# Kernel tuning notes

Hardware: AMD Instinct MI355X
Metric: run time of the kernel (lower is better)

Reference implementation:

```python
import jax, jax.numpy as jnp
import numpy as np

B, C, M = 4, 4096, 2048
H, D = 16, 128
S = D // 2


def setup_inputs() -> dict:
    key = jax.random.key(0)
    k1, k2, k3, k4 = jax.random.split(key, 4)
    x = jax.random.normal(k1, (B, C, M), dtype=jnp.float32)
    q = jax.random.normal(k2, (B, H, C, D), dtype=jnp.float32)
    k = jax.random.normal(k3, (B, H, C, D), dtype=jnp.float32)
    embed_weight = jax.random.normal(k4, (H, M), dtype=jnp.float32)
    pos_weight = jnp.ones((H,), dtype=jnp.float32)
    # buffer: theta = 10000 ** (-arange(0, D, 2) / D), shape [S]
    theta_steps = jnp.power(10000.0, -jnp.arange(0, D, 2, dtype=jnp.float32) / D)
    return {"x": x, "q": q, "k": k, "embed_weight": embed_weight,
            "pos_weight": pos_weight, "theta_steps": theta_steps}


def _rotate(proj_BHCD, cos_BHCS, sin_BHCS):
    # Givens matrix per (b,h,c,s): [[cos, sin], [-sin, cos]], applied as
    # rot_j = sum_i G[i,j] * p_i  =>  r0 = cos*p0 - sin*p1 ; r1 = sin*p0 + cos*p1
    Bs, Hs, Cs, Ds = proj_BHCD.shape
    p = proj_BHCD.reshape(Bs, Hs, Cs, Ds // 2, 2)
    p0, p1 = p[..., 0], p[..., 1]
    r0 = cos_BHCS * p0 - sin_BHCS * p1
    r1 = sin_BHCS * p0 + cos_BHCS * p1
    return jnp.stack([r0, r1], axis=-1).reshape(Bs, Hs, Cs, Ds)


def reference(x, q, k, embed_weight, pos_weight, theta_steps):
    # data-dependent position: input_BHC = x @ embed_weight per head
    input_BHC = jnp.einsum('bcm,hm->bhc', x, embed_weight)
    Cn = x.shape[1]
    pos_BHC = pos_weight[None, :, None] * jnp.arange(Cn, dtype=x.dtype) + input_BHC
    ang_BHCS = pos_BHC[..., None] * theta_steps  # [B,H,C,S]
    cos_t, sin_t = jnp.cos(ang_BHCS), jnp.sin(ang_BHCS)
    rot_q = _rotate(q, cos_t, sin_t)
    rot_k = _rotate(k, cos_t, sin_t)
    return jnp.stack([rot_q, rot_k], axis=0)  # [2,B,H,C,D]
```

## Files before the change

kernel.cpp:

```cpp
#include <hip/hip_runtime.h>

#define Bn 4
#define Cn 4096
#define Mn 2048
#define Hn 16
#define Dn 128
#define Sn 64

typedef float f4 __attribute__((ext_vector_type(4)));

__global__ __launch_bounds__(1024, 4) void pos_kernel(
    const float* __restrict__ x,
    const float* __restrict__ W,
    const float* __restrict__ pw,
    float* __restrict__ pos)
{
    __shared__ __align__(16) float Wl[Hn * Mn];
    __shared__ float posbuf[Hn][33];

    const int t = threadIdx.x;

    const float4* W4  = (const float4*)W;
    float4*       Wl4 = (float4*)Wl;
#pragma unroll
    for (int kk = 0; kk < 8; ++kk)
        Wl4[kk * 1024 + t] = W4[kk * 1024 + t];
    __syncthreads();

    const int wid  = t >> 6;
    const int lane = t & 63;
    const int row0 = blockIdx.x * 32;
    const int b    = row0 >> 12;
    const int c0   = row0 & 4095;
    const int r0   = row0 + wid * 2;

    const float4* x4 = (const float4*)x;
    const size_t  xb = (size_t)r0 * (Mn / 4);

    float acc0[16], acc1[16];
#pragma unroll
    for (int h = 0; h < Hn; ++h) { acc0[h] = 0.0f; acc1[h] = 0.0f; }

    float4 xa = x4[xb + lane];
    float4 xc = x4[xb + 512 + lane];
#pragma unroll
    for (int j = 0; j < 8; ++j) {
        float4 na, nc;
        if (j < 7) {
            na = x4[xb + (j + 1) * 64 + lane];
            nc = x4[xb + 512 + (j + 1) * 64 + lane];
        }
#pragma unroll
        for (int h = 0; h < Hn; ++h) {
            const float4 wv = Wl4[h * 512 + j * 64 + lane];
            acc0[h] += xa.x * wv.x; acc0[h] += xa.y * wv.y;
            acc0[h] += xa.z * wv.z; acc0[h] += xa.w * wv.w;
            acc1[h] += xc.x * wv.x; acc1[h] += xc.y * wv.y;
            acc1[h] += xc.z * wv.z; acc1[h] += xc.w * wv.w;
        }
        if (j < 7) { xa = na; xc = nc; }
    }

    float vals[32];
#pragma unroll
    for (int h = 0; h < Hn; ++h) { vals[h] = acc0[h]; vals[16 + h] = acc1[h]; }

#pragma unroll
    for (int s = 0; s < 5; ++s) {
        const int m = 1 << s;
        const int nout = 16 >> s;
        const bool up = (lane & m) != 0;
#pragma unroll
        for (int k = 0; k < 16; ++k) {
            if (k < nout) {
                float a = vals[2 * k], bb = vals[2 * k + 1];
                float mine = up ? bb : a;
                float oth  = up ? a  : bb;
                vals[k] = mine + __shfl_xor(oth, m);
            }
        }
    }
    const float tot = vals[0] + __shfl_xor(vals[0], 32);

    if (lane < 32) {
        const int h = lane & 15;
        const int r = (lane >> 4) & 1;
        posbuf[h][wid * 2 + r] = tot;
    }
    __syncthreads();

    if (t < 512) {
        const int h  = t >> 5;
        const int cc = t & 31;
        const int c  = c0 + cc;
        pos[((size_t)(b * Hn + h)) * Cn + c] = pw[h] * (float)c + posbuf[h][cc];
    }
}

__global__ __launch_bounds__(256) void rot_kernel(
    const float* __restrict__ q,
    const float* __restrict__ k,
    const float* __restrict__ theta,
    const float* __restrict__ pos,
    float* __restrict__ out)
{
    const size_t tid = (size_t)blockIdx.x * 256 + threadIdx.x;
    const int sp = (int)(tid & 31);
    const size_t row = tid >> 5;

    const float p = pos[row];
    const float2 th = ((const float2*)theta)[sp];

    constexpr float inv2pi = 0.15915494309189535f;
    float r0 = p * th.x * inv2pi;
    float r1 = p * th.y * inv2pi;
    r0 = r0 - floorf(r0);
    r1 = r1 - floorf(r1);
    const float cs0 = __builtin_amdgcn_cosf(r0);
    const float sn0 = __builtin_amdgcn_sinf(r0);
    const float cs1 = __builtin_amdgcn_cosf(r1);
    const float sn1 = __builtin_amdgcn_sinf(r1);

    const f4* q4 = (const f4*)q;
    const f4* k4 = (const f4*)k;
    f4* o4 = (f4*)out;
    const size_t idx = row * 32 + sp;
    const size_t half = (size_t)Bn * Hn * Cn * 32;

    const f4 qv = q4[idx];
    f4 ov;
    ov.x = cs0 * qv.x - sn0 * qv.y;
    ov.y = sn0 * qv.x + cs0 * qv.y;
    ov.z = cs1 * qv.z - sn1 * qv.w;
    ov.w = sn1 * qv.z + cs1 * qv.w;
    __builtin_nontemporal_store(ov, o4 + idx);

    const f4 kv = k4[idx];
    f4 ok;
    ok.x = cs0 * kv.x - sn0 * kv.y;
    ok.y = sn0 * kv.x + cs0 * kv.y;
    ok.z = cs1 * kv.z - sn1 * kv.w;
    ok.w = sn1 * kv.z + cs1 * kv.w;
    __builtin_nontemporal_store(ok, o4 + idx + half);
}

extern "C" void kernel_launch(void* const* d_in, const int* in_sizes, int n_in,
                              void* d_out, int out_size, void* d_ws, size_t ws_size,
                              hipStream_t stream) {
    const float* x     = (const float*)d_in[0];
    const float* q     = (const float*)d_in[1];
    const float* k     = (const float*)d_in[2];
    const float* W     = (const float*)d_in[3];
    const float* pw    = (const float*)d_in[4];
    const float* theta = (const float*)d_in[5];
    float* out = (float*)d_out;
    float* pos = (float*)d_ws;

    pos_kernel<<<512, 1024, 0, stream>>>(x, W, pw, pos);

    rot_kernel<<<32768, 256, 0, stream>>>(q, k, theta, pos, out);
}
```

Before: 553.2 us.

## Process four rows per wavefront in pos kernel and halve block count

Each wavefront in the position-projection kernel now handles four x rows instead of two, so each shared-memory W read feeds four rows. The grid is halved, which halves the number of times the 128KB W matrix is staged into LDS. The W layout in LDS is rearranged to be j-major, and the shuffle reduction is extended by one stage so it covers 64 values. The cost is more accumulator registers, which can reduce occupancy, and fewer blocks (256) to spread across the CUs.

```diff
diff --git a/kernel.cpp b/kernel.cpp
--- a/kernel.cpp
+++ b/kernel.cpp
@@ -16,62 +16,82 @@
     float* __restrict__ pos)
 {
     __shared__ __align__(16) float Wl[Hn * Mn];
-    __shared__ float posbuf[Hn][33];
+    __shared__ float posbuf[Hn][65];
 
     const int t = threadIdx.x;
 
     const float4* W4  = (const float4*)W;
     float4*       Wl4 = (float4*)Wl;
 #pragma unroll
-    for (int kk = 0; kk < 8; ++kk)
-        Wl4[kk * 1024 + t] = W4[kk * 1024 + t];
+    for (int kk = 0; kk < 8; ++kk) {
+        const int idx = kk * 1024 + t;
+        const int h   = idx >> 9;
+        const int m4  = idx & 511;
+        const int j   = m4 >> 6;
+        const int ln  = m4 & 63;
+        Wl4[(j * 16 + h) * 64 + ln] = W4[idx];
+    }
     __syncthreads();
 
     const int wid  = t >> 6;
     const int lane = t & 63;
-    const int row0 = blockIdx.x * 32;
+    const int row0 = blockIdx.x * 64;
     const int b    = row0 >> 12;
     const int c0   = row0 & 4095;
-    const int r0   = row0 + wid * 2;
+    const int r0   = row0 + wid * 4;
 
     const float4* x4 = (const float4*)x;
     const size_t  xb = (size_t)r0 * (Mn / 4);
 
-    float acc0[16], acc1[16];
+    float acc[4][16];
 #pragma unroll
-    for (int h = 0; h < Hn; ++h) { acc0[h] = 0.0f; acc1[h] = 0.0f; }
+    for (int r = 0; r < 4; ++r)
+#pragma unroll
+        for (int h = 0; h < Hn; ++h) acc[r][h] = 0.0f;
 
-    float4 xa = x4[xb + lane];
-    float4 xc = x4[xb + 512 + lane];
+    float4 cur[4];
+#pragma unroll
+    for (int r = 0; r < 4; ++r) cur[r] = x4[xb + (size_t)r * 512 + lane];
+
 #pragma unroll
     for (int j = 0; j < 8; ++j) {
-        float4 na, nc;
+        float4 nxt[4];
         if (j < 7) {
-            na = x4[xb + (j + 1) * 64 + lane];
-            nc = x4[xb + 512 + (j + 1) * 64 + lane];
+#pragma unroll
+            for (int r = 0; r < 4; ++r)
+                nxt[r] = x4[xb + (size_t)r * 512 + (j + 1) * 64 + lane];
         }
+        const float4* wj = Wl4 + j * 1024;
 #pragma unroll
         for (int h = 0; h < Hn; ++h) {
-            const float4 wv = Wl4[h * 512 + j * 64 + lane];
-            acc0[h] += xa.x * wv.x; acc0[h] += xa.y * wv.y;
-            acc0[h] += xa.z * wv.z; acc0[h] += xa.w * wv.w;
-            acc1[h] += xc.x * wv.x; acc1[h] += xc.y * wv.y;
-            acc1[h] += xc.z * wv.z; acc1[h] += xc.w * wv.w;
+            const float4 wv = wj[h * 64 + lane];
+#pragma unroll
+            for (int r = 0; r < 4; ++r) {
+                acc[r][h] += cur[r].x * wv.x;
+                acc[r][h] += cur[r].y * wv.y;
+                acc[r][h] += cur[r].z * wv.z;
+                acc[r][h] += cur[r].w * wv.w;
+            }
         }
-        if (j < 7) { xa = na; xc = nc; }
+        if (j < 7) {
+#pragma unroll
+            for (int r = 0; r < 4; ++r) cur[r] = nxt[r];
+        }
     }
 
-    float vals[32];
+    float vals[64];
 #pragma unroll
-    for (int h = 0; h < Hn; ++h) { vals[h] = acc0[h]; vals[16 + h] = acc1[h]; }
+    for (int r = 0; r < 4; ++r)
+#pragma unroll
+        for (int h = 0; h < Hn; ++h) vals[r * 16 + h] = acc[r][h];
 
 #pragma unroll
-    for (int s = 0; s < 5; ++s) {
+    for (int s = 0; s < 6; ++s) {
         const int m = 1 << s;
-        const int nout = 16 >> s;
+        const int nout = 32 >> s;
         const bool up = (lane & m) != 0;
 #pragma unroll
-        for (int k = 0; k < 16; ++k) {
+        for (int k = 0; k < 32; ++k) {
             if (k < nout) {
                 float a = vals[2 * k], bb = vals[2 * k + 1];
                 float mine = up ? bb : a;
@@ -80,18 +100,16 @@
             }
         }
     }
-    const float tot = vals[0] + __shfl_xor(vals[0], 32);
-
-    if (lane < 32) {
+    {
         const int h = lane & 15;
-        const int r = (lane >> 4) & 1;
-        posbuf[h][wid * 2 + r] = tot;
+        const int r = lane >> 4;
+        posbuf[h][wid * 4 + r] = vals[0];
     }
     __syncthreads();
 
-    if (t < 512) {
-        const int h  = t >> 5;
-        const int cc = t & 31;
+    {
+        const int h  = t >> 6;
+        const int cc = t & 63;
         const int c  = c0 + cc;
         pos[((size_t)(b * Hn + h)) * Cn + c] = pw[h] * (float)c + posbuf[h][cc];
     }
@@ -156,7 +174,7 @@
     float* out = (float*)d_out;
     float* pos = (float*)d_ws;
 
-    pos_kernel<<<512, 1024, 0, stream>>>(x, W, pw, pos);
+    pos_kernel<<<256, 1024, 0, stream>>>(x, W, pw, pos);
 
     rot_kernel<<<32768, 256, 0, stream>>>(q, k, theta, pos, out);
 }
```

Result: faster. 526.1 us (-4.9%).
